# Kernel tuning notes

Hardware: AMD Instinct MI355X
Metric: run time of the kernel (lower is better)

The kernel has to match this reference:

```python
import jax, jax.numpy as jnp
import numpy as np
from jax import lax

B = 2048                 # scenes = agent/av/env nodes
K_OTH, K_LANE = 16, 32
N_OTH, N_LANE = B * K_OTH, B * K_LANE
T_HIST, T_AV, T_PRED = 20, 20, 30
H = 25                   # LSTM hidden
NH, FO = 5, 5            # GAT heads / out feats


def _lstm(x, Wih, Whh, b, h0, c0):
    # x: [T, N, I]; torch gate order i, f, g, o
    def step(carry, xt):
        h, c = carry
        g = xt @ Wih.T + h @ Whh.T + b
        i, f, gg, o = jnp.split(g, 4, axis=-1)
        c = jax.nn.sigmoid(f) * c + jax.nn.sigmoid(i) * jnp.tanh(gg)
        h = jax.nn.sigmoid(o) * jnp.tanh(c)
        return (h, c), h
    (h, c), hs = lax.scan(step, (h0, c0), x)
    return hs, h, c


def _seg_mean(x, idx, n):
    s = jax.ops.segment_sum(x, idx, num_segments=n)
    cnt = jax.ops.segment_sum(jnp.ones((x.shape[0],), x.dtype), idx, num_segments=n)
    return s / cnt[:, None]


def _gat(src_feat, dst_feat, src_idx, dst_idx, W, al, ar, b, n_dst):
    # DGL GATConv: shared fc for src/dst, leaky_relu(0.2), edge-softmax per dst node/head
    fs = (src_feat @ W.T).reshape(-1, NH, FO)   # [Ns, NH, FO]
    fd = (dst_feat @ W.T).reshape(-1, NH, FO)   # [Nd, NH, FO]
    el = (fs * al).sum(-1)                      # [Ns, NH]
    er = (fd * ar).sum(-1)                      # [Nd, NH]
    e = jax.nn.leaky_relu(el[src_idx] + er[dst_idx], negative_slope=0.2)  # [E, NH]
    emax = jax.ops.segment_max(e, dst_idx, num_segments=n_dst)
    ee = jnp.exp(e - emax[dst_idx])
    a = ee / jax.ops.segment_sum(ee, dst_idx, num_segments=n_dst)[dst_idx]
    out = jax.ops.segment_sum(fs[src_idx] * a[:, :, None], dst_idx, num_segments=n_dst)
    return out + b.reshape(NH, FO)              # [Nd, NH, FO]


def setup_inputs():
    key = jax.random.key(0)
    ks = iter(jax.random.split(key, 48))
    def rn(shape, s=1.0):
        return jax.random.normal(next(ks), shape, jnp.float32) * s
    def lstm_p(pre, i):
        return {pre + '_Wih': rn((4 * H, i), 0.2), pre + '_Whh': rn((4 * H, H), 0.2), pre + '_b': rn((4 * H,), 0.1)}
    def gat_p(pre):
        return {pre + '_W': rn((NH * FO, H), 0.2), pre + '_al': rn((NH, FO), 0.2), pre + '_ar': rn((NH, FO), 0.2), pre + '_b': rn((NH * FO,), 0.1)}
    inp = {
        'agent_state': rn((B, T_HIST + T_PRED, 2)),
        'av_state': rn((B, T_AV, 2)),
        'others_state': rn((N_OTH, T_AV, 2)),
        'lane_state': rn((N_LANE, T_AV, 2)),
    }
    inp.update(lstm_p('ag', 2)); inp.update(lstm_p('av', 2)); inp.update(lstm_p('ot', 2)); inp.update(lstm_p('de', 1))
    inp['lin_W'] = rn((2, H), 0.2); inp['lin_b'] = rn((2,), 0.1)
    inp.update(gat_p('gav')); inp.update(gat_p('got')); inp.update(gat_p('gln'))
    inp['others_dst'] = jnp.arange(N_OTH, dtype=jnp.int32) // K_OTH   # env id of each 'others' node
    inp['lane_dst'] = jnp.arange(N_LANE, dtype=jnp.int32) // K_LANE   # env id of each 'lane' node
    return inp


def reference(agent_state, av_state, others_state, lane_state,
              ag_Wih, ag_Whh, ag_b, av_Wih, av_Whh, av_b, ot_Wih, ot_Whh, ot_b,
              de_Wih, de_Whh, de_b, lin_W, lin_b,
              gav_W, gav_al, gav_ar, gav_b, got_W, got_al, got_ar, got_b,
              gln_W, gln_al, gln_ar, gln_b, others_dst, lane_dst):
    Bn = agent_state.shape[0]
    dt = agent_state.dtype
    z = lambda n: jnp.zeros((n, H), dt)

    # --- LSTM encoders (time-major, like torch nn.LSTM) ---
    agent = jnp.transpose(agent_state[:, :T_HIST, :], (1, 0, 2))
    _, ag_h, ag_c = _lstm(agent, ag_Wih, ag_Whh, ag_b, z(Bn), z(Bn))
    _, _, av_c = _lstm(jnp.transpose(av_state, (1, 0, 2)), av_Wih, av_Whh, av_b, z(Bn), z(Bn))
    no, nl = others_state.shape[0], lane_state.shape[0]
    _, _, ot_c = _lstm(jnp.transpose(others_state, (1, 0, 2)), ot_Wih, ot_Whh, ot_b, z(no), z(no))
    # NOTE: original code encodes lanes with the *agent* encoder (faithful to source bug)
    _, _, ln_c = _lstm(jnp.transpose(lane_state, (1, 0, 2)), ag_Wih, ag_Whh, ag_b, z(nl), z(nl))

    # --- update_all(copy_u, mean) ---
    env_agent_info = ag_c                       # exactly one agent per env -> mean == identity
    env_lane_info = _seg_mean(ln_c, lane_dst, Bn)

    # --- HeteroGraphConv of 3 GATConvs, aggregate='mean' ---
    e_av = _gat(av_c, env_agent_info, jnp.arange(Bn), jnp.arange(Bn), gav_W, gav_al, gav_ar, gav_b, Bn)
    e_ot = _gat(ot_c, env_agent_info, jnp.arange(no), others_dst, got_W, got_al, got_ar, got_b, Bn)
    e_ln = _gat(ln_c, env_agent_info, jnp.arange(nl), lane_dst, gln_W, gln_al, gln_ar, gln_b, Bn)
    env_code = ((e_av + e_ot + e_ln) / 3.0).reshape(Bn, NH * FO)   # [B, 25]

    # --- LSTM decoder over t = arange(0, 3, 0.1) ---
    t = jnp.broadcast_to(jnp.arange(0.0, 3.0, 0.1, dtype=dt).reshape(T_PRED, 1, 1), (T_PRED, Bn, 1))
    hs, _, _ = _lstm(t, de_Wih, de_Whh, de_b, ag_h, ag_c + env_code)
    predict = jnp.transpose(hs @ lin_W.T + lin_b, (1, 0, 2))       # [B, 30, 2]
    return predict, env_lane_info
```

## Files before the change

kernel.cpp:

```cpp
#include <hip/hip_runtime.h>


typedef __attribute__((ext_vector_type(8))) short s16x8;
typedef __attribute__((ext_vector_type(4))) float fx4;

__device__ __forceinline__ float frcp(float x) { return __builtin_amdgcn_rcpf(x); }
__device__ __forceinline__ float fsig(float x) { return frcp(1.f + __expf(-x)); }
__device__ __forceinline__ float ftanh(float x) { return 1.f - 2.f * frcp(1.f + __expf(2.f * x)); }

__device__ __forceinline__ float exp2p(float x) { float r; asm("v_exp_f32 %0, %1"  : "=v"(r) : "v"(x)); return r; }
__device__ __forceinline__ float exp2m(float x) { float r; asm("v_exp_f32 %0, -%1" : "=v"(r) : "v"(x)); return r; }

__device__ __forceinline__ unsigned bfhi(float f) {
    unsigned b = __float_as_uint(f);
    return (b + 0x7FFFu + ((b >> 16) & 1u)) >> 16;
}
__device__ __forceinline__ float bfval(unsigned h) { return __uint_as_float(h << 16); }

__device__ __forceinline__ void buildB2(const float* L, int q, int n, s16x8& hi, s16x8& lo) {
    float f[8];
#pragma unroll
    for (int e = 0; e < 8; ++e) f[e] = L[(8 * q + e) * 17 + n];
    union { unsigned w[4]; s16x8 v; } H, Lo;
#pragma unroll
    for (int i = 0; i < 4; ++i) {
        unsigned hw;
        asm("v_cvt_pk_bf16_f32 %0, %1, %2" : "=v"(hw) : "v"(f[2 * i]), "v"(f[2 * i + 1]));
        const float r0 = f[2 * i]     - __uint_as_float(hw << 16);
        const float r1 = f[2 * i + 1] - __uint_as_float(hw & 0xFFFF0000u);
        unsigned lw;
        asm("v_cvt_pk_bf16_f32 %0, %1, %2" : "=v"(lw) : "v"(r0), "v"(r1));
        H.w[i] = hw; Lo.w[i] = lw;
    }
    hi = H.v; lo = Lo.v;
}

__global__ __launch_bounds__(64, 1) void enc_kernel(
    const float* __restrict__ agent, const float* __restrict__ av,
    const float* __restrict__ oth,   const float* __restrict__ lane,
    const float* __restrict__ agWih, const float* __restrict__ agWhh, const float* __restrict__ agB,
    const float* __restrict__ avWih, const float* __restrict__ avWhh, const float* __restrict__ avB,
    const float* __restrict__ otWih, const float* __restrict__ otWhh, const float* __restrict__ otB,
    float* __restrict__ ws)
{
    __shared__ float hlds[32 * 17];

    const int l = threadIdx.x & 63;
    const int n = l & 15;
    const int q = l >> 4;
    float* L = hlds;

    const int g0 = blockIdx.x;
    int task;
    if (g0 < 128) task = 0;
    else if (g0 < 256) task = 1;
    else if (g0 < 2304) task = 2;
    else task = 3;

    const float* Whh; const float* Wih; const float* Bp;
    if (task == 1)      { Wih = avWih; Whh = avWhh; Bp = avB; }
    else if (task == 2) { Wih = otWih; Whh = otWhh; Bp = otB; }
    else                { Wih = agWih; Whh = agWhh; Bp = agB; }

    const int node = g0 * 16 + n;
    const float* xp;
    if (task == 0)      xp = agent + node * 100;
    else if (task == 1) xp = av   + (node - 2048)  * 40;
    else if (task == 2) xp = oth  + (node - 4096)  * 40;
    else                xp = lane + (node - 36864) * 40;

    float xv[10];
#pragma unroll
    for (int s = 0; s < 5; ++s) {
        float2 t2 = *reinterpret_cast<const float2*>(xp + 2 * (5 * q + s));
        xv[2 * s] = t2.x; xv[2 * s + 1] = t2.y;
    }

    const float L2E = 1.4426950408889634f;
    s16x8 Ahi[7], Alo[7];
#pragma unroll
    for (int T = 0; T < 7; ++T) {
        const int p = 16 * T + n;
        const int r = p & 3;
        const int u = p >> 2;
        int row = r * 25 + u;
        if (row > 99) row = 99;
        const float sc = (r == 2) ? 2.f * L2E : L2E;
        float w[8];
        if (q < 3) {
            const float* src = Whh + row * 25 + 8 * q;
#pragma unroll
            for (int e = 0; e < 8; ++e) w[e] = src[e] * sc;
        } else {
            w[0] = Whh[row * 25 + 24] * sc;
            w[1] = Wih[row * 2] * sc;
            w[2] = Wih[row * 2 + 1] * sc;
            w[3] = Bp[row] * sc;
            w[4] = w[5] = w[6] = w[7] = 0.f;
        }
#pragma unroll
        for (int e = 0; e < 8; ++e) {
            unsigned h = bfhi(w[e]);
            unsigned lo = bfhi(w[e] - bfval(h));
            Ahi[T][e] = (short)h;
            Alo[T][e] = (short)lo;
        }
    }

#pragma unroll
    for (int T = 0; T < 6; ++T) L[(4 * T + q) * 17 + n] = 0.f;
    if (q == 0) {
        L[24 * 17 + n] = 0.f;
        L[25 * 17 + n] = xv[0];
        L[26 * 17 + n] = xv[1];
    }
    if (q == 3) L[27 * 17 + n] = 1.f;
    L[(28 + q) * 17 + n] = 0.f;
    __builtin_amdgcn_wave_barrier();

    s16x8 Bh, Bl;
    buildB2(L, q, n, Bh, Bl);

    float c[7], hv[7];
#pragma unroll
    for (int T = 0; T < 7; ++T) { c[T] = 0.f; hv[T] = 0.f; }

    const fx4 zero4 = {0.f, 0.f, 0.f, 0.f};
    const float TL2E = 2.f * L2E;

#pragma unroll 1
    for (int tt = 0; tt < 4; ++tt) {
#pragma unroll
        for (int s = 0; s < 5; ++s) {
            fx4 acc[7];
#pragma unroll
            for (int T = 0; T < 7; ++T) {
                fx4 a = __builtin_amdgcn_mfma_f32_16x16x32_bf16(Ahi[T], Bh, zero4, 0, 0, 0);
                a = __builtin_amdgcn_mfma_f32_16x16x32_bf16(Ahi[T], Bl, a, 0, 0, 0);
                acc[T] = __builtin_amdgcn_mfma_f32_16x16x32_bf16(Alo[T], Bh, a, 0, 0, 0);
            }
#pragma unroll
            for (int T = 0; T < 7; ++T) {
                const float A  = exp2m(acc[T][0]);
                const float Bv = exp2m(acc[T][1]);
                const float Cv = exp2p(acc[T][2]);
                const float D  = exp2m(acc[T][3]);
                const float a1 = 1.f + A;
                const float b1 = 1.f + Bv;
                const float c1 = 1.f + Cv;
                const float cm = Cv - 1.f;
                const float P  = a1 * c1;
                const float t0 = cm * b1;
                const float num = fmaf(c[T], P, t0);
                const float den = P * b1;
                c[T] = num * frcp(den);
                const float E  = exp2p(c[T] * TL2E);
                const float e1 = 1.f + E;
                const float em = E - 1.f;
                const float d1 = 1.f + D;
                hv[T] = em * frcp(d1 * e1);
            }
            const bool lastStep = (tt == 3) && (s == 4);
            if (!lastStep) {
#pragma unroll
                for (int T = 0; T < 6; ++T) L[(4 * T + q) * 17 + n] = hv[T];
                if (q == 0) L[24 * 17 + n] = hv[6];
                if (s < 4) {
                    if (q == tt) {
                        L[25 * 17 + n] = xv[2 * (s + 1)];
                        L[26 * 17 + n] = xv[2 * (s + 1) + 1];
                    }
                } else {
                    if (q == tt + 1) {
                        L[25 * 17 + n] = xv[0];
                        L[26 * 17 + n] = xv[1];
                    }
                }
                __builtin_amdgcn_wave_barrier();
                buildB2(L, q, n, Bh, Bl);
            }
        }
    }

    float* dst_c; float* dst_h = nullptr;
    if (task == 0)      { dst_h = ws + node * 25; dst_c = ws + 51200 + node * 25; }
    else if (task == 1) dst_c = ws + 102400 + (node - 2048) * 25;
    else if (task == 2) dst_c = ws + 153600 + (node - 4096) * 25;
    else                dst_c = ws + 972800 + (node - 36864) * 25;
#pragma unroll
    for (int T = 0; T < 7; ++T) {
        const int u = 4 * T + q;
        if (u < 25) {
            dst_c[u] = c[T];
            if (task == 0) dst_h[u] = hv[T];
        }
    }
}

__global__ __launch_bounds__(256) void gat_kernel(
    const float* __restrict__ ws,
    const float* __restrict__ gavW, const float* __restrict__ gavAl, const float* __restrict__ gavAr, const float* __restrict__ gavB,
    const float* __restrict__ gotW, const float* __restrict__ gotAl, const float* __restrict__ gotAr, const float* __restrict__ gotB,
    const float* __restrict__ glnW, const float* __restrict__ glnAl, const float* __restrict__ glnAr, const float* __restrict__ glnB,
    float* __restrict__ envcode, float* __restrict__ lane_out)
{
    __shared__ float X[50 * 25];
    __shared__ float F[52 * 25];
    __shared__ float er[10];
    __shared__ float Eo[16 * 5];
    __shared__ float El[32 * 5];

    const int tid = threadIdx.x;
    const int b = blockIdx.x;
    const float* agc = ws + 51200;
    const float* avc = ws + 102400;
    const float* otc = ws + 153600;
    const float* lnc = ws + 972800;

    for (int i = tid; i < 1250; i += 256) {
        int r = i / 25, k = i - r * 25;
        float v;
        if (r == 0)      v = agc[b * 25 + k];
        else if (r == 1) v = avc[b * 25 + k];
        else if (r < 18) v = otc[(b * 16 + (r - 2)) * 25 + k];
        else             v = lnc[(b * 32 + (r - 18)) * 25 + k];
        X[i] = v;
    }
    __syncthreads();

    for (int d = tid; d < 1300; d += 256) {
        int row = d / 25, o = d - row * 25;
        const float* W; const float* xs;
        if (row == 0)      { W = gavW; xs = &X[1 * 25]; }
        else if (row == 1) { W = gavW; xs = &X[0]; }
        else if (row == 2) { W = gotW; xs = &X[0]; }
        else if (row == 3) { W = glnW; xs = &X[0]; }
        else if (row < 20) { W = gotW; xs = &X[(2 + row - 4) * 25]; }
        else               { W = glnW; xs = &X[(18 + row - 20) * 25]; }
        float acc = 0.f;
#pragma unroll
        for (int k = 0; k < 25; ++k) acc += W[o * 25 + k] * xs[k];
        F[row * 25 + o] = acc;
    }
    __syncthreads();

    if (tid < 10) {
        int conv = tid / 5, nn = tid - conv * 5;
        const float* ar = conv ? glnAr : gotAr;
        const float* fd = &F[(2 + conv) * 25];
        float acc = 0.f;
#pragma unroll
        for (int f = 0; f < 5; ++f) acc += fd[nn * 5 + f] * ar[nn * 5 + f];
        er[tid] = acc;
    }
    __syncthreads();

    for (int d = tid; d < 240; d += 256) {
        if (d < 80) {
            int i = d / 5, nn = d - i * 5;
            const float* fsrow = &F[(4 + i) * 25];
            float acc = er[nn];
#pragma unroll
            for (int f = 0; f < 5; ++f) acc += fsrow[nn * 5 + f] * gotAl[nn * 5 + f];
            Eo[d] = (acc > 0.f) ? acc : 0.2f * acc;
        } else {
            int d2 = d - 80;
            int i = d2 / 5, nn = d2 - i * 5;
            const float* fsrow = &F[(20 + i) * 25];
            float acc = er[5 + nn];
#pragma unroll
            for (int f = 0; f < 5; ++f) acc += fsrow[nn * 5 + f] * glnAl[nn * 5 + f];
            El[d2] = (acc > 0.f) ? acc : 0.2f * acc;
        }
    }
    __syncthreads();

    if (tid < 10) {
        int conv = tid / 5, nn = tid - conv * 5;
        if (conv == 0) {
            float m = -1e30f;
            for (int i = 0; i < 16; ++i) m = fmaxf(m, Eo[i * 5 + nn]);
            float s = 0.f;
            for (int i = 0; i < 16; ++i) s += __expf(Eo[i * 5 + nn] - m);
            float inv = frcp(s);
            for (int i = 0; i < 16; ++i) Eo[i * 5 + nn] = __expf(Eo[i * 5 + nn] - m) * inv;
        } else {
            float m = -1e30f;
            for (int i = 0; i < 32; ++i) m = fmaxf(m, El[i * 5 + nn]);
            float s = 0.f;
            for (int i = 0; i < 32; ++i) s += __expf(El[i * 5 + nn] - m);
            float inv = frcp(s);
            for (int i = 0; i < 32; ++i) El[i * 5 + nn] = __expf(El[i * 5 + nn] - m) * inv;
        }
    }
    __syncthreads();

    if (tid < 25) {
        const int o = tid, nn = o / 5;
        float v_av = F[o] + gavB[o];
        float s = 0.f;
        for (int i = 0; i < 16; ++i) s += Eo[i * 5 + nn] * F[(4 + i) * 25 + o];
        float v_ot = s + gotB[o];
        s = 0.f;
        for (int i = 0; i < 32; ++i) s += El[i * 5 + nn] * F[(20 + i) * 25 + o];
        float v_ln = s + glnB[o];
        envcode[b * 25 + o] = (v_av + v_ot + v_ln) * (1.f / 3.f);
        float m = 0.f;
        for (int i = 0; i < 32; ++i) m += X[(18 + i) * 25 + o];
        lane_out[b * 25 + o] = m * (1.f / 32.f);
    }
}

__global__ __launch_bounds__(256) void dec_kernel(
    const float* __restrict__ ws,
    const float* __restrict__ deWih, const float* __restrict__ deWhh, const float* __restrict__ deB,
    const float* __restrict__ linW,  const float* __restrict__ linB,
    float* __restrict__ out)
{
    __shared__ float hbuf[8][28];
    const int tid  = threadIdx.x;
    const int lane = tid & 63;
    const int half = lane >> 5;
    const int u    = lane & 31;
    const int u2   = (u < 25) ? u : 0;
    const bool act = (u < 25);
    const int wglob = (blockIdx.x * 256 + tid) >> 6;
    const int b = wglob * 2 + half;
    const int envloc = ((tid >> 6) << 1) + half;

    float U[4][25], Wi[4], Bb[4];
#pragma unroll
    for (int r = 0; r < 4; ++r) {
        const int row = u2 + 25 * r;
#pragma unroll
        for (int k = 0; k < 25; ++k) U[r][k] = deWhh[row * 25 + k];
        Wi[r] = deWih[row];
        Bb[r] = deB[row];
    }
    const int j = u & 1;
    float lw[25];
#pragma unroll
    for (int k = 0; k < 25; ++k) lw[k] = linW[j * 25 + k];
    const float lb = linB[j];

    const float* agh = ws;
    const float* agc = ws + 51200;
    const float* env = ws + 2611200;

    float h[25];
#pragma unroll
    for (int k = 0; k < 25; ++k) h[k] = agh[b * 25 + k];
    float c_own = agc[b * 25 + u2] + env[b * 25 + u2];

    for (int t = 0; t < 30; ++t) {
        const float tt = 0.1f * (float)t;
        float g[4];
#pragma unroll
        for (int r = 0; r < 4; ++r) {
            float acc = Bb[r] + Wi[r] * tt;
#pragma unroll
            for (int k = 0; k < 25; ++k) acc += U[r][k] * h[k];
            g[r] = acc;
        }
        const float iv = fsig(g[0]);
        const float fv = fsig(g[1]);
        const float gv = ftanh(g[2]);
        const float ov = fsig(g[3]);
        c_own = fv * c_own + iv * gv;
        const float ho = ov * ftanh(c_own);
        if (act) hbuf[envloc][u] = ho;
        __builtin_amdgcn_wave_barrier();
#pragma unroll
        for (int k = 0; k < 25; ++k) h[k] = hbuf[envloc][k];
        float ov2 = lb;
#pragma unroll
        for (int k = 0; k < 25; ++k) ov2 += lw[k] * h[k];
        if (u < 2) out[b * 60 + t * 2 + u] = ov2;
    }
}

extern "C" void kernel_launch(void* const* d_in, const int* in_sizes, int n_in,
                              void* d_out, int out_size, void* d_ws, size_t ws_size,
                              hipStream_t stream)
{
    const float* agent = (const float*)d_in[0];
    const float* av    = (const float*)d_in[1];
    const float* oth   = (const float*)d_in[2];
    const float* lane  = (const float*)d_in[3];
    const float* agWih = (const float*)d_in[4];
    const float* agWhh = (const float*)d_in[5];
    const float* agB   = (const float*)d_in[6];
    const float* avWih = (const float*)d_in[7];
    const float* avWhh = (const float*)d_in[8];
    const float* avB   = (const float*)d_in[9];
    const float* otWih = (const float*)d_in[10];
    const float* otWhh = (const float*)d_in[11];
    const float* otB   = (const float*)d_in[12];
    const float* deWih = (const float*)d_in[13];
    const float* deWhh = (const float*)d_in[14];
    const float* deB   = (const float*)d_in[15];
    const float* linW  = (const float*)d_in[16];
    const float* linB  = (const float*)d_in[17];
    const float* gavW  = (const float*)d_in[18];
    const float* gavAl = (const float*)d_in[19];
    const float* gavAr = (const float*)d_in[20];
    const float* gavB  = (const float*)d_in[21];
    const float* gotW  = (const float*)d_in[22];
    const float* gotAl = (const float*)d_in[23];
    const float* gotAr = (const float*)d_in[24];
    const float* gotB  = (const float*)d_in[25];
    const float* glnW  = (const float*)d_in[26];
    const float* glnAl = (const float*)d_in[27];
    const float* glnAr = (const float*)d_in[28];
    const float* glnB  = (const float*)d_in[29];

    float* out = (float*)d_out;
    float* ws  = (float*)d_ws;

    enc_kernel<<<6400, 64, 0, stream>>>(agent, av, oth, lane,
                                        agWih, agWhh, agB,
                                        avWih, avWhh, avB,
                                        otWih, otWhh, otB, ws);

    gat_kernel<<<2048, 256, 0, stream>>>(ws,
                                         gavW, gavAl, gavAr, gavB,
                                         gotW, gotAl, gotAr, gotB,
                                         glnW, glnAl, glnAr, glnB,
                                         ws + 2611200, out + 122880);

    dec_kernel<<<256, 256, 0, stream>>>(ws, deWih, deWhh, deB, linW, linB, out);
}
```

Baseline: 129.7 us.

## Fuse decoder LSTM into GAT kernel, one scene per block

Merges the decoder LSTM into the GAT kernel so each block first computes its scene's env code in shared memory and then runs the 30-step decoder with its first wave. This removes one kernel launch and the global round trip of the env code. The decoder now uses only one wave per 256-thread block, so most threads sit idle for the serial recurrence, and only about half of that wave's lanes (u < 25 in the lower half) do useful gate work instead of two scenes per wave. That lowers decoder parallelism and occupancy.

After: 170.1 us. 1.31x slower.

```diff
diff --git a/kernel.cpp b/kernel.cpp
--- a/kernel.cpp
+++ b/kernel.cpp
@@ -197,18 +197,22 @@
     }
 }
 
-__global__ __launch_bounds__(256) void gat_kernel(
+__global__ __launch_bounds__(256) void gat_dec_kernel(
     const float* __restrict__ ws,
     const float* __restrict__ gavW, const float* __restrict__ gavAl, const float* __restrict__ gavAr, const float* __restrict__ gavB,
     const float* __restrict__ gotW, const float* __restrict__ gotAl, const float* __restrict__ gotAr, const float* __restrict__ gotB,
     const float* __restrict__ glnW, const float* __restrict__ glnAl, const float* __restrict__ glnAr, const float* __restrict__ glnB,
-    float* __restrict__ envcode, float* __restrict__ lane_out)
+    const float* __restrict__ deWih, const float* __restrict__ deWhh, const float* __restrict__ deB,
+    const float* __restrict__ linW,  const float* __restrict__ linB,
+    float* __restrict__ out, float* __restrict__ lane_out)
 {
     __shared__ float X[50 * 25];
     __shared__ float F[52 * 25];
     __shared__ float er[10];
     __shared__ float Eo[16 * 5];
     __shared__ float El[32 * 5];
+    __shared__ float envc[25];
+    __shared__ float dbuf[28];
 
     const int tid = threadIdx.x;
     const int b = blockIdx.x;
@@ -304,29 +308,19 @@
         s = 0.f;
         for (int i = 0; i < 32; ++i) s += El[i * 5 + nn] * F[(20 + i) * 25 + o];
         float v_ln = s + glnB[o];
-        envcode[b * 25 + o] = (v_av + v_ot + v_ln) * (1.f / 3.f);
+        envc[o] = (v_av + v_ot + v_ln) * (1.f / 3.f);
         float m = 0.f;
         for (int i = 0; i < 32; ++i) m += X[(18 + i) * 25 + o];
         lane_out[b * 25 + o] = m * (1.f / 32.f);
-    }
-}
-
-__global__ __launch_bounds__(256) void dec_kernel(
-    const float* __restrict__ ws,
-    const float* __restrict__ deWih, const float* __restrict__ deWhh, const float* __restrict__ deB,
-    const float* __restrict__ linW,  const float* __restrict__ linB,
-    float* __restrict__ out)
-{
-    __shared__ float hbuf[8][28];
-    const int tid  = threadIdx.x;
+        if (o >= 25 - 3) dbuf[o + 3] = 0.f;
+    }
+    __syncthreads();
+
+    if (tid >= 64) return;
     const int lane = tid & 63;
-    const int half = lane >> 5;
     const int u    = lane & 31;
     const int u2   = (u < 25) ? u : 0;
-    const bool act = (u < 25);
-    const int wglob = (blockIdx.x * 256 + tid) >> 6;
-    const int b = wglob * 2 + half;
-    const int envloc = ((tid >> 6) << 1) + half;
+    const bool act = (u < 25) && (lane < 32);
 
     float U[4][25], Wi[4], Bb[4];
 #pragma unroll
@@ -344,13 +338,10 @@
     const float lb = linB[j];
 
     const float* agh = ws;
-    const float* agc = ws + 51200;
-    const float* env = ws + 2611200;
-
     float h[25];
 #pragma unroll
     for (int k = 0; k < 25; ++k) h[k] = agh[b * 25 + k];
-    float c_own = agc[b * 25 + u2] + env[b * 25 + u2];
+    float c_own = agc[b * 25 + u2] + envc[u2];
 
     for (int t = 0; t < 30; ++t) {
         const float tt = 0.1f * (float)t;
@@ -368,14 +359,14 @@
         const float ov = fsig(g[3]);
         c_own = fv * c_own + iv * gv;
         const float ho = ov * ftanh(c_own);
-        if (act) hbuf[envloc][u] = ho;
+        if (act) dbuf[u] = ho;
         __builtin_amdgcn_wave_barrier();
 #pragma unroll
-        for (int k = 0; k < 25; ++k) h[k] = hbuf[envloc][k];
+        for (int k = 0; k < 25; ++k) h[k] = dbuf[k];
         float ov2 = lb;
 #pragma unroll
         for (int k = 0; k < 25; ++k) ov2 += lw[k] * h[k];
-        if (u < 2) out[b * 60 + t * 2 + u] = ov2;
+        if (lane < 2) out[b * 60 + t * 2 + lane] = ov2;
     }
 }
 
@@ -422,11 +413,10 @@
                                         avWih, avWhh, avB,
                                         otWih, otWhh, otB, ws);
 
-    gat_kernel<<<2048, 256, 0, stream>>>(ws,
-                                         gavW, gavAl, gavAr, gavB,
-                                         gotW, gotAl, gotAr, gotB,
-                                         glnW, glnAl, glnAr, glnB,
-                                         ws + 2611200, out + 122880);
-
-    dec_kernel<<<256, 256, 0, stream>>>(ws, deWih, deWhh, deB, linW, linB, out);
+    gat_dec_kernel<<<2048, 256, 0, stream>>>(ws,
+                                             gavW, gavAl, gavAr, gavB,
+                                             gotW, gotAl, gotAr, gotB,
+                                             glnW, glnAl, glnAr, glnB,
+                                             deWih, deWhh, deB, linW, linB,
+                                             out, out + 122880);
 }
```
